# Performance work log

Hardware: AMD Instinct MI355X
Metric: run time of the kernel (lower is better)

Reference implementation:

```python
import jax, jax.numpy as jnp
import numpy as np

B, T, IN, H, OUT = 4096, 256, 2, 50, 2


def _rnn_layer(x, W_ih, W_hh, b_ih, b_hh):
    # x: [B, T, F] -> out: [B, T, H]. Elman RNN: h_t = tanh(W_ih x_t + b_ih + W_hh h_{t-1} + b_hh)
    pre = jnp.einsum('btf,hf->bth', x, W_ih) + b_ih + b_hh  # input projection hoisted out of scan
    h0 = jnp.zeros((x.shape[0], W_hh.shape[0]), dtype=x.dtype)

    def step(h, pre_t):
        h = jnp.tanh(pre_t + h @ W_hh.T)
        return h, h

    _, hs = jax.lax.scan(step, h0, jnp.swapaxes(pre, 0, 1))  # scan over time: [T, B, H]
    return jnp.swapaxes(hs, 0, 1)


def setup_inputs() -> dict:
    key = jax.random.key(0)
    ks = jax.random.split(key, 16)
    s_in = 1.0 / np.sqrt(H)  # torch nn.RNN init: U(-1/sqrt(H), 1/sqrt(H))

    def u(k, shape):
        return jax.random.uniform(k, shape, jnp.float32, -s_in, s_in)

    return {
        'x': jax.random.normal(ks[0], (B, T, IN), jnp.float32),
        'W_ih1': u(ks[1], (H, IN)), 'W_hh1': u(ks[2], (H, H)), 'b_ih1': u(ks[3], (H,)), 'b_hh1': u(ks[4], (H,)),
        'W_ih2': u(ks[5], (H, H)), 'W_hh2': u(ks[6], (H, H)), 'b_ih2': u(ks[7], (H,)), 'b_hh2': u(ks[8], (H,)),
        'W_ih3': u(ks[9], (H, H)), 'W_hh3': u(ks[10], (H, H)), 'b_ih3': u(ks[11], (H,)), 'b_hh3': u(ks[12], (H,)),
        'fc_w': u(ks[13], (OUT, H)), 'fc_b': u(ks[14], (OUT,)),
    }


def reference(x, W_ih1, W_hh1, b_ih1, b_hh1, W_ih2, W_hh2, b_ih2, b_hh2,
              W_ih3, W_hh3, b_ih3, b_hh3, fc_w, fc_b):
    out = _rnn_layer(x, W_ih1, W_hh1, b_ih1, b_hh1)
    out = _rnn_layer(out, W_ih2, W_hh2, b_ih2, b_hh2)
    out = _rnn_layer(out, W_ih3, W_hh3, b_ih3, b_hh3)
    return out[:, -1, :] @ fc_w.T + fc_b  # [B, OUT]
```

## Files before the change

kernel.cpp:

```cpp
#include <hip/hip_runtime.h>
#include <hip/hip_fp16.h>

namespace {

constexpr int T_STEPS = 256;
constexpr int HD = 50;
constexpr int HP = 64;
constexpr int KST = 88;
constexpr int KSTS = 72;
constexpr int BT = 16;
constexpr int NTHR = 768;
constexpr int XST = 34;
constexpr int LAY_SH = BT * KST;
constexpr int SLOT_SH = 3 * LAY_SH;

typedef __attribute__((ext_vector_type(8))) _Float16 f16x8;
typedef __attribute__((ext_vector_type(4))) float f32x4;

__device__ __forceinline__ unsigned short f2h(float x) {
  __half h = __float2half(x);
  return *reinterpret_cast<unsigned short*>(&h);
}
__device__ __forceinline__ float h2f(unsigned short u) {
  __half h;
  *reinterpret_cast<unsigned short*>(&h) = u;
  return __half2float(h);
}

#define MFMA16 __builtin_amdgcn_mfma_f32_16x16x32_f16

__device__ __forceinline__ void barrier_nodrain() {
  asm volatile("s_barrier" ::: "memory");
}

__global__ __launch_bounds__(NTHR, 3) void rnn3_kernel(
    const float* __restrict__ x,
    const float* __restrict__ Wih1, const float* __restrict__ Whh1,
    const float* __restrict__ bih1, const float* __restrict__ bhh1,
    const float* __restrict__ Wih2, const float* __restrict__ Whh2,
    const float* __restrict__ bih2, const float* __restrict__ bhh2,
    const float* __restrict__ Wih3, const float* __restrict__ Whh3,
    const float* __restrict__ bih3, const float* __restrict__ bhh3,
    const float* __restrict__ fcw, const float* __restrict__ fcb,
    float* __restrict__ out) {
  __shared__ unsigned short hbuf[3 * SLOT_SH];
  __shared__ float xls[T_STEPS][XST];
  __shared__ unsigned short scr[HP * KSTS];

  const int tid = threadIdx.x;
  const int w = tid >> 6;
  const int myL = w >> 2;
  const int wv = w & 3;
  const int lane = tid & 63;
  const int quad = lane >> 4;
  const int l15 = lane & 15;
  const int b0 = blockIdx.x * BT;

  {
    unsigned int* hz = reinterpret_cast<unsigned int*>(hbuf);
    const int n = 3 * SLOT_SH / 2;
    for (int i = tid; i < n; i += NTHR) hz[i] = 0u;
  }
  for (int idx = tid; idx < BT * T_STEPS; idx += NTHR) {
    int b = idx >> 8, t = idx & 255;
    float2 v = *reinterpret_cast<const float2*>(x + (size_t)(b0 + b) * (T_STEPS * 2) + 2 * t);
    xls[t][2 * b] = v.x;
    xls[t][2 * b + 1] = v.y;
  }

  const float* mats[5] = {Whh1, Wih2, Whh2, Wih3, Whh3};
  constexpr int matL[5] = {0, 1, 1, 2, 2};
  constexpr int matS[5] = {0, 0, 1, 0, 1};
  f16x8 wA[2][2];
#pragma unroll
  for (int sl = 0; sl < 2; ++sl)
#pragma unroll
    for (int ks = 0; ks < 2; ++ks) wA[sl][ks] = f16x8(0);

  const int arow = 16 * wv + l15;
#pragma unroll
  for (int m = 0; m < 5; ++m) {
    __syncthreads();
    const float* W = mats[m];
    for (int idx = tid; idx < HP * HP; idx += NTHR) {
      int i = idx >> 6, k = idx & 63;
      float v = (i < HD && k < HD) ? W[i * HD + k] : 0.0f;
      scr[i * KSTS + k] = f2h(v);
    }
    __syncthreads();
    if (myL == matL[m]) {
      const int sl = matS[m];
      const unsigned short* ph = &scr[arow * KSTS + 8 * quad];
      wA[sl][0] = *reinterpret_cast<const f16x8*>(ph);
      wA[sl][1] = *reinterpret_cast<const f16x8*>(ph + 32);
    }
  }

  const int ic = 16 * wv + 4 * quad;
  const float* bi = (myL == 0) ? bih1 : (myL == 1) ? bih2 : bih3;
  const float* bh = (myL == 0) ? bhh1 : (myL == 1) ? bhh2 : bhh3;
  float wx0[4], wx1[4];
  f32x4 bsv;
#pragma unroll
  for (int r = 0; r < 4; ++r) {
    int i = ic + r;
    bool v = i < HD;
    bsv[r] = v ? (bi[i] + bh[i]) : 0.0f;
    wx0[r] = (v && myL == 0) ? Wih1[i * 2 + 0] : 0.0f;
    wx1[r] = (v && myL == 0) ? Wih1[i * 2 + 1] : 0.0f;
  }

  const int selfBuf = myL;
  const int crossBuf = (myL > 0) ? myL - 1 : 0;
  const int ldsOff = l15 * KST + 8 * quad;

  const unsigned short* sbase = hbuf + selfBuf * LAY_SH + ldsOff;
  const unsigned short* cbase = hbuf + crossBuf * LAY_SH + ldsOff;
  unsigned short* wbase = hbuf + myL * LAY_SH + l15 * KST + ic;

  f16x8 pfC0 = f16x8(0), pfC1 = f16x8(0);
  float2 xpf;

  __syncthreads();
  xpf = *reinterpret_cast<const float2*>(&xls[0][2 * l15]);

  auto core = [&](int s, int wr, int rd) {
    f16x8 bS0 = *reinterpret_cast<const f16x8*>(sbase + rd * SLOT_SH);
    f16x8 bS1 = *reinterpret_cast<const f16x8*>(sbase + rd * SLOT_SH + 32);
    f32x4 c;
    if (myL == 0) {
      f32x4 ci;
#pragma unroll
      for (int r = 0; r < 4; ++r) ci[r] = fmaf(wx1[r], xpf.y, fmaf(wx0[r], xpf.x, bsv[r]));
      c = MFMA16(wA[0][0], bS0, ci, 0, 0, 0);
      c = MFMA16(wA[0][1], bS1, c, 0, 0, 0);
    } else {
      c = MFMA16(wA[0][0], pfC0, bsv, 0, 0, 0);
      c = MFMA16(wA[0][1], pfC1, c, 0, 0, 0);
      c = MFMA16(wA[1][0], bS0, c, 0, 0, 0);
      c = MFMA16(wA[1][1], bS1, c, 0, 0, 0);
    }
    if (wv != 3) {
      float d[4];
#pragma unroll
      for (int r = 0; r < 4; ++r) {
        float xr = __builtin_amdgcn_fmed3f(c[r], -11.0f, 11.0f);
        d[r] = __expf(2.0f * xr) + 1.0f;
      }
      float p01 = d[0] * d[1], p23 = d[2] * d[3];
      float rp = __builtin_amdgcn_rcpf(p01 * p23);
      float q01 = rp * p23, q23 = rp * p01;
      float iv[4] = {q01 * d[1], q01 * d[0], q23 * d[3], q23 * d[2]};
      unsigned short ht[4];
#pragma unroll
      for (int r = 0; r < 4; ++r) ht[r] = f2h(fmaf(-2.0f, iv[r], 1.0f));
      unsigned int h01 = (unsigned int)ht[0] | ((unsigned int)ht[1] << 16);
      unsigned int h23 = (unsigned int)ht[2] | ((unsigned int)ht[3] << 16);
      *reinterpret_cast<uint2*>(wbase + wr * SLOT_SH) = make_uint2(h01, h23);
    } else {
      float x0 = __builtin_amdgcn_fmed3f(c[0], -11.0f, 11.0f);
      float x1 = __builtin_amdgcn_fmed3f(c[1], -11.0f, 11.0f);
      float d0 = __expf(2.0f * x0) + 1.0f;
      float d1 = __expf(2.0f * x1) + 1.0f;
      float rp = __builtin_amdgcn_rcpf(d0 * d1);
      unsigned short t0 = f2h(fmaf(-2.0f, rp * d1, 1.0f));
      unsigned short t1 = f2h(fmaf(-2.0f, rp * d0, 1.0f));
      if (quad == 0) {
        *reinterpret_cast<uint2*>(wbase + wr * SLOT_SH) =
            make_uint2((unsigned)t0 | ((unsigned)t1 << 16), 0u);
      }
    }
    if (myL > 0) {
      pfC0 = *reinterpret_cast<const f16x8*>(cbase + rd * SLOT_SH);
      pfC1 = *reinterpret_cast<const f16x8*>(cbase + rd * SLOT_SH + 32);
    } else {
      xpf = *reinterpret_cast<const float2*>(&xls[(s + 1) & 255][2 * l15]);
    }
  };

  auto actOf = [&](int s) {
    return (myL == 0) ? (s < T_STEPS)
         : (myL == 1) ? (s >= 2 && s < T_STEPS + 2)
                      : (s >= 4);
  };

  auto stepB = [&](int s, int wr, int rd, bool act) {
    if (act) {
      core(s, wr, rd);
    } else if (myL > 0) {
      pfC0 = *reinterpret_cast<const f16x8*>(cbase + rd * SLOT_SH);
      pfC1 = *reinterpret_cast<const f16x8*>(cbase + rd * SLOT_SH + 32);
    }
    __syncthreads();
  };

  for (int s = 0; s < 4; ++s) stepB(s, s % 3, (s + 2) % 3, actOf(s));
  for (int sb = 4; sb < 256; sb += 3) {
    core(sb + 0, 1, 0); barrier_nodrain();
    core(sb + 1, 2, 1); barrier_nodrain();
    core(sb + 2, 0, 2); barrier_nodrain();
  }
  __syncthreads();
  for (int s = 256; s < 260; ++s) stepB(s, s % 3, (s + 2) % 3, actOf(s));

  if (tid < BT * 2) {
    int b = tid >> 1, o = tid & 1;
    const unsigned short* h3 = hbuf + 1 * SLOT_SH + 2 * LAY_SH + b * KST;
    float acc = fcb[o];
    for (int i = 0; i < HD; ++i) acc += fcw[o * HD + i] * h2f(h3[i]);
    out[(size_t)(b0 + b) * 2 + o] = acc;
  }
}

}

extern "C" void kernel_launch(void* const* d_in, const int* in_sizes, int n_in,
                              void* d_out, int out_size, void* d_ws, size_t ws_size,
                              hipStream_t stream) {
  const float* x = (const float*)d_in[0];
  const float* Wih1 = (const float*)d_in[1];
  const float* Whh1 = (const float*)d_in[2];
  const float* bih1 = (const float*)d_in[3];
  const float* bhh1 = (const float*)d_in[4];
  const float* Wih2 = (const float*)d_in[5];
  const float* Whh2 = (const float*)d_in[6];
  const float* bih2 = (const float*)d_in[7];
  const float* bhh2 = (const float*)d_in[8];
  const float* Wih3 = (const float*)d_in[9];
  const float* Whh3 = (const float*)d_in[10];
  const float* bih3 = (const float*)d_in[11];
  const float* bhh3 = (const float*)d_in[12];
  const float* fcw = (const float*)d_in[13];
  const float* fcb = (const float*)d_in[14];

  rnn3_kernel<<<4096 / BT, NTHR, 0, stream>>>(x, Wih1, Whh1, bih1, bhh1,
                                              Wih2, Whh2, bih2, bhh2,
                                              Wih3, Whh3, bih3, bhh3,
                                              fcw, fcb, (float*)d_out);
}
```

Baseline: 192.2 us.

## Halve waves per block, giving each wave two 16-row output tiles

Cuts the block from 12 to 6 waves, so each layer uses two waves and each wave computes two 16-row M-tiles of the hidden state per step. This halves the waves taking part in every per-timestep barrier and lets each wave reuse its loaded B fragments across two MFMA chains. The factor of 2 inside tanh is folded into the fp16 weights and biases to save a multiply. In exchange each wave carries more serial MFMA and transcendental work per step, and min-blocks drops to 2, which changes occupancy.

```diff
diff --git a/kernel.cpp b/kernel.cpp
--- a/kernel.cpp
+++ b/kernel.cpp
@@ -9,7 +9,7 @@
 constexpr int KST = 88;
 constexpr int KSTS = 72;
 constexpr int BT = 16;
-constexpr int NTHR = 768;
+constexpr int NTHR = 384;
 constexpr int XST = 34;
 constexpr int LAY_SH = BT * KST;
 constexpr int SLOT_SH = 3 * LAY_SH;
@@ -33,7 +33,7 @@
   asm volatile("s_barrier" ::: "memory");
 }
 
-__global__ __launch_bounds__(NTHR, 3) void rnn3_kernel(
+__global__ __launch_bounds__(NTHR, 2) void rnn3_kernel(
     const float* __restrict__ x,
     const float* __restrict__ Wih1, const float* __restrict__ Whh1,
     const float* __restrict__ bih1, const float* __restrict__ bhh1,
@@ -49,8 +49,8 @@
 
   const int tid = threadIdx.x;
   const int w = tid >> 6;
-  const int myL = w >> 2;
-  const int wv = w & 3;
+  const int myL = w >> 1;
+  const int mh = w & 1;
   const int lane = tid & 63;
   const int quad = lane >> 4;
   const int l15 = lane & 15;
@@ -71,44 +71,49 @@
   const float* mats[5] = {Whh1, Wih2, Whh2, Wih3, Whh3};
   constexpr int matL[5] = {0, 1, 1, 2, 2};
   constexpr int matS[5] = {0, 0, 1, 0, 1};
-  f16x8 wA[2][2];
+  f16x8 wA[2][2][2];
 #pragma unroll
   for (int sl = 0; sl < 2; ++sl)
 #pragma unroll
-    for (int ks = 0; ks < 2; ++ks) wA[sl][ks] = f16x8(0);
-
-  const int arow = 16 * wv + l15;
+    for (int mt = 0; mt < 2; ++mt)
+#pragma unroll
+      for (int ks = 0; ks < 2; ++ks) wA[sl][mt][ks] = f16x8(0);
+
 #pragma unroll
   for (int m = 0; m < 5; ++m) {
     __syncthreads();
     const float* W = mats[m];
     for (int idx = tid; idx < HP * HP; idx += NTHR) {
       int i = idx >> 6, k = idx & 63;
-      float v = (i < HD && k < HD) ? W[i * HD + k] : 0.0f;
+      float v = (i < HD && k < HD) ? 2.0f * W[i * HD + k] : 0.0f;
       scr[i * KSTS + k] = f2h(v);
     }
     __syncthreads();
     if (myL == matL[m]) {
       const int sl = matS[m];
-      const unsigned short* ph = &scr[arow * KSTS + 8 * quad];
-      wA[sl][0] = *reinterpret_cast<const f16x8*>(ph);
-      wA[sl][1] = *reinterpret_cast<const f16x8*>(ph + 32);
-    }
-  }
-
-  const int ic = 16 * wv + 4 * quad;
+#pragma unroll
+      for (int mt = 0; mt < 2; ++mt) {
+        const unsigned short* ph = &scr[(32 * mh + 16 * mt + l15) * KSTS + 8 * quad];
+        wA[sl][mt][0] = *reinterpret_cast<const f16x8*>(ph);
+        wA[sl][mt][1] = *reinterpret_cast<const f16x8*>(ph + 32);
+      }
+    }
+  }
+
   const float* bi = (myL == 0) ? bih1 : (myL == 1) ? bih2 : bih3;
   const float* bh = (myL == 0) ? bhh1 : (myL == 1) ? bhh2 : bhh3;
-  float wx0[4], wx1[4];
-  f32x4 bsv;
-#pragma unroll
-  for (int r = 0; r < 4; ++r) {
-    int i = ic + r;
-    bool v = i < HD;
-    bsv[r] = v ? (bi[i] + bh[i]) : 0.0f;
-    wx0[r] = (v && myL == 0) ? Wih1[i * 2 + 0] : 0.0f;
-    wx1[r] = (v && myL == 0) ? Wih1[i * 2 + 1] : 0.0f;
-  }
+  f32x4 bsv[2];
+  float wx0[2][4], wx1[2][4];
+#pragma unroll
+  for (int mt = 0; mt < 2; ++mt)
+#pragma unroll
+    for (int r = 0; r < 4; ++r) {
+      int i = 32 * mh + 16 * mt + 4 * quad + r;
+      bool v = i < HD;
+      bsv[mt][r] = v ? 2.0f * (bi[i] + bh[i]) : 0.0f;
+      wx0[mt][r] = (v && myL == 0) ? 2.0f * Wih1[i * 2 + 0] : 0.0f;
+      wx1[mt][r] = (v && myL == 0) ? 2.0f * Wih1[i * 2 + 1] : 0.0f;
+    }
 
   const int selfBuf = myL;
   const int crossBuf = (myL > 0) ? myL - 1 : 0;
@@ -116,7 +121,7 @@
 
   const unsigned short* sbase = hbuf + selfBuf * LAY_SH + ldsOff;
   const unsigned short* cbase = hbuf + crossBuf * LAY_SH + ldsOff;
-  unsigned short* wbase = hbuf + myL * LAY_SH + l15 * KST + ic;
+  unsigned short* wbase0 = hbuf + myL * LAY_SH + l15 * KST + 32 * mh + 4 * quad;
 
   f16x8 pfC0 = f16x8(0), pfC1 = f16x8(0);
   float2 xpf;
@@ -127,47 +132,58 @@
   auto core = [&](int s, int wr, int rd) {
     f16x8 bS0 = *reinterpret_cast<const f16x8*>(sbase + rd * SLOT_SH);
     f16x8 bS1 = *reinterpret_cast<const f16x8*>(sbase + rd * SLOT_SH + 32);
-    f32x4 c;
+    f32x4 cm[2];
     if (myL == 0) {
-      f32x4 ci;
-#pragma unroll
-      for (int r = 0; r < 4; ++r) ci[r] = fmaf(wx1[r], xpf.y, fmaf(wx0[r], xpf.x, bsv[r]));
-      c = MFMA16(wA[0][0], bS0, ci, 0, 0, 0);
-      c = MFMA16(wA[0][1], bS1, c, 0, 0, 0);
+#pragma unroll
+      for (int mt = 0; mt < 2; ++mt) {
+        f32x4 ci;
+#pragma unroll
+        for (int r = 0; r < 4; ++r)
+          ci[r] = fmaf(wx1[mt][r], xpf.y, fmaf(wx0[mt][r], xpf.x, bsv[mt][r]));
+        f32x4 c = MFMA16(wA[0][mt][0], bS0, ci, 0, 0, 0);
+        cm[mt] = MFMA16(wA[0][mt][1], bS1, c, 0, 0, 0);
+      }
     } else {
-      c = MFMA16(wA[0][0], pfC0, bsv, 0, 0, 0);
-      c = MFMA16(wA[0][1], pfC1, c, 0, 0, 0);
-      c = MFMA16(wA[1][0], bS0, c, 0, 0, 0);
-      c = MFMA16(wA[1][1], bS1, c, 0, 0, 0);
-    }
-    if (wv != 3) {
-      float d[4];
-#pragma unroll
-      for (int r = 0; r < 4; ++r) {
-        float xr = __builtin_amdgcn_fmed3f(c[r], -11.0f, 11.0f);
-        d[r] = __expf(2.0f * xr) + 1.0f;
-      }
-      float p01 = d[0] * d[1], p23 = d[2] * d[3];
-      float rp = __builtin_amdgcn_rcpf(p01 * p23);
-      float q01 = rp * p23, q23 = rp * p01;
-      float iv[4] = {q01 * d[1], q01 * d[0], q23 * d[3], q23 * d[2]};
-      unsigned short ht[4];
-#pragma unroll
-      for (int r = 0; r < 4; ++r) ht[r] = f2h(fmaf(-2.0f, iv[r], 1.0f));
-      unsigned int h01 = (unsigned int)ht[0] | ((unsigned int)ht[1] << 16);
-      unsigned int h23 = (unsigned int)ht[2] | ((unsigned int)ht[3] << 16);
-      *reinterpret_cast<uint2*>(wbase + wr * SLOT_SH) = make_uint2(h01, h23);
-    } else {
-      float x0 = __builtin_amdgcn_fmed3f(c[0], -11.0f, 11.0f);
-      float x1 = __builtin_amdgcn_fmed3f(c[1], -11.0f, 11.0f);
-      float d0 = __expf(2.0f * x0) + 1.0f;
-      float d1 = __expf(2.0f * x1) + 1.0f;
-      float rp = __builtin_amdgcn_rcpf(d0 * d1);
-      unsigned short t0 = f2h(fmaf(-2.0f, rp * d1, 1.0f));
-      unsigned short t1 = f2h(fmaf(-2.0f, rp * d0, 1.0f));
-      if (quad == 0) {
-        *reinterpret_cast<uint2*>(wbase + wr * SLOT_SH) =
-            make_uint2((unsigned)t0 | ((unsigned)t1 << 16), 0u);
+#pragma unroll
+      for (int mt = 0; mt < 2; ++mt) {
+        f32x4 c = MFMA16(wA[0][mt][0], pfC0, bsv[mt], 0, 0, 0);
+        c = MFMA16(wA[0][mt][1], pfC1, c, 0, 0, 0);
+        c = MFMA16(wA[1][mt][0], bS0, c, 0, 0, 0);
+        cm[mt] = MFMA16(wA[1][mt][1], bS1, c, 0, 0, 0);
+      }
+    }
+#pragma unroll
+    for (int mt = 0; mt < 2; ++mt) {
+      if (mh == 1 && mt == 1) {
+        float x0 = __builtin_amdgcn_fmed3f(cm[1][0], -22.0f, 22.0f);
+        float x1 = __builtin_amdgcn_fmed3f(cm[1][1], -22.0f, 22.0f);
+        float d0 = __expf(x0) + 1.0f;
+        float d1 = __expf(x1) + 1.0f;
+        float rp = __builtin_amdgcn_rcpf(d0 * d1);
+        unsigned short t0 = f2h(fmaf(-2.0f, rp * d1, 1.0f));
+        unsigned short t1 = f2h(fmaf(-2.0f, rp * d0, 1.0f));
+        if (quad == 0) {
+          *reinterpret_cast<uint2*>(wbase0 + 16 + wr * SLOT_SH) =
+              make_uint2((unsigned)t0 | ((unsigned)t1 << 16), 0u);
+        }
+      } else {
+        float d[4];
+#pragma unroll
+        for (int r = 0; r < 4; ++r) {
+          float xr = __builtin_amdgcn_fmed3f(cm[mt][r], -22.0f, 22.0f);
+          d[r] = __expf(xr) + 1.0f;
+        }
+        float p01 = d[0] * d[1], p23 = d[2] * d[3];
+        float rp = __builtin_amdgcn_rcpf(p01 * p23);
+        float q01 = rp * p23, q23 = rp * p01;
+        float iv[4] = {q01 * d[1], q01 * d[0], q23 * d[3], q23 * d[2]};
+        unsigned short ht[4];
+#pragma unroll
+        for (int r = 0; r < 4; ++r) ht[r] = f2h(fmaf(-2.0f, iv[r], 1.0f));
+        unsigned int h01 = (unsigned int)ht[0] | ((unsigned int)ht[1] << 16);
+        unsigned int h23 = (unsigned int)ht[2] | ((unsigned int)ht[3] << 16);
+        *reinterpret_cast<uint2*>(wbase0 + 16 * mt + wr * SLOT_SH) =
+            make_uint2(h01, h23);
       }
     }
     if (myL > 0) {
```

After: 216.0 us. 1.12x slower.
